# Optimization experiments

Measured on AMD Instinct MI355X. Metric: run time of the kernel, lower is better.

Reference implementation:

```python
import jax, jax.numpy as jnp
import numpy as np

N = 64
K_CHEB = 5
EPS = 1e-5

# db4 decomposition filters (scaling_filter.mat Lo_D / Hi_D, length 8)
_LO = np.array([-0.010597401784997278, 0.032883011666982945, 0.030841381835986965,
                -0.18703481171888114, -0.02798376941698385, 0.6308807679295904,
                0.7148465705525415, 0.23037781330885523], dtype=np.float32)
_HI = np.array([-0.23037781330885523, 0.7148465705525415, -0.6308807679295904,
                -0.02798376941698385, 0.18703481171888114, 0.030841381835986965,
                0.032883011666982945, -0.010597401784997278], dtype=np.float32)
# torch stores np.flip(filters) and Conv2d does cross-correlation -> use flipped taps here too
_KERN = np.stack([_LO[::-1], _HI[::-1]])[:, None, None, :].copy()  # [2,1,1,8]


def _wavelet_step(x):
    # x: [B, C, 1, W]; circular pad 3 each side, depthwise len-8 conv, stride 2
    p = 3  # filter_length // 2 - 1
    xp = jnp.concatenate([x[..., -p:], x, x[..., :p]], axis=-1)
    b, c, h, wp = xp.shape
    out = jax.lax.conv_general_dilated(
        xp.reshape(b * c, 1, h, wp), jnp.asarray(_KERN), (1, 2), 'VALID',
        dimension_numbers=('NCHW', 'OIHW', 'NCHW'))
    out = out.reshape(b, c, 2, h, -1)
    return out[:, :, 0], out[:, :, 1]  # (approx, detail)


def _cbam(x, fc1, fc2, sa_w):
    # x: [B, 657, 1, 64]; channel attention then spatial attention
    def mlp(v):  # v: [B, C, 1, 1]
        h = jax.nn.relu(jnp.einsum('oc,bchw->bohw', fc1, v))
        return jnp.einsum('oc,bchw->bohw', fc2, h)
    avg = x.mean(axis=(2, 3), keepdims=True)
    mx = x.max(axis=(2, 3), keepdims=True)
    x = x * jax.nn.sigmoid(mlp(avg) + mlp(mx))
    s = jnp.concatenate([x.mean(axis=1, keepdims=True), x.max(axis=1, keepdims=True)], axis=1)
    sa = jax.nn.sigmoid(jax.lax.conv_general_dilated(
        s, sa_w, (1, 1), ((3, 3), (3, 3)), dimension_numbers=('NCHW', 'OIHW', 'NCHW')))
    return x * sa


def _global_edge_weight(w_tril, mask):
    xs, ys = np.tril_indices(N)
    E = jnp.zeros((N, N), w_tril.dtype).at[xs, ys].set(w_tril)
    E = E + E.T - jnp.diag(jnp.diag(E))
    return (E * mask).reshape(-1)


def _norm_adj(edges, w):
    # PyG NewSGConv.norm: add remaining self-loops (fill=1), deg from |w|, sym normalize
    row, col = edges[0], edges[1]
    has_self = jnp.zeros((N,), w.dtype).at[row].add(jnp.where(row == col, 1.0, 0.0)) > 0
    w_self = jnp.where(has_self, 0.0, 1.0).astype(w.dtype)
    deg = jnp.zeros((N,), w.dtype).at[row].add(jnp.abs(w)) + w_self
    dsafe = jnp.where(deg > 0, deg, 1.0)
    dinv = jnp.where(deg > 0, jax.lax.rsqrt(dsafe), 0.0)
    norm = dinv[row] * w * dinv[col]
    A = jnp.zeros((N, N), w.dtype).at[col, row].add(norm)  # out[i] = sum_j A[i,j] x[j]
    return A + jnp.diag(dinv * w_self * dinv)


def _gcn_block(x, A, W, b, g, be):
    # x: [B, N, C_in]; K-hop SGConv propagation, linear, train-mode batchnorm over (B, N)
    for _ in range(K_CHEB):
        x = jnp.einsum('ij,bjc->bic', A, x)
    x = x @ W.T + b
    mean = x.mean(axis=(0, 1))
    var = x.var(axis=(0, 1))
    return (x - mean) * jax.lax.rsqrt(var + EPS) * g + be


def _classify(x, W1, b1, g, be, W2, b2):
    out = x.reshape(x.shape[0], -1) @ W1.T + b1
    out = (out - out.mean(0)) * jax.lax.rsqrt(out.var(0) + EPS) * g + be
    return jax.nn.log_softmax(out @ W2.T + b2, axis=1)


def _forward(x, local_graph_weight, global_mask, ca_fc1, ca_fc2, sa_conv, edge_weight_tril,
             ld_W, ld_b, ld_g, ld_be, ld1_W, ld1_b, ld1_g, ld1_be,
             d_W, d_b, d_g, d_be, d1_W, d1_b, d1_g, d1_be,
             cls_W1, cls_b1, cls_g, cls_be, cls_W2, cls_b2, edges):
    xc = jnp.transpose(x, (0, 3, 2, 1))        # [B, 657, 1, 64]
    xc = _cbam(xc, ca_fc1, ca_fc2, sa_conv)
    xh = jnp.transpose(xc, (0, 3, 2, 1))       # [B, 64, 1, 657]
    # fi = floor(log2(200)) = 7 -> 4 decomposition levels: 657->328->164->82->41
    out1, _gamma = _wavelet_step(xh)
    out2, _beta = _wavelet_step(out1)
    out3, _alpha = _wavelet_step(out2)
    delta, _theta = _wavelet_step(out3)        # [B, 64, 1, 41]
    delta = delta[:, :, 0, :]                  # squeeze -> [B, 64, 41]
    gw = _global_edge_weight(edge_weight_tril, global_mask)
    A_loc = _norm_adj(edges, local_graph_weight)
    A_glb = _norm_adj(edges, gw)
    lf = _gcn_block(delta, A_loc, ld_W, ld_b, ld_g, ld_be)
    lf = _gcn_block(lf, A_loc, ld1_W, ld1_b, ld1_g, ld1_be)
    gf = _gcn_block(delta, A_glb, d_W, d_b, d_g, d_be)
    gf = _gcn_block(gf, A_glb, d1_W, d1_b, d1_g, d1_be)
    feat = jnp.concatenate([lf.mean(-1, keepdims=True), gf.mean(-1, keepdims=True)], axis=2)  # [B,64,2]
    return _classify(feat, cls_W1, cls_b1, cls_g, cls_be, cls_W2, cls_b2)


def setup_inputs() -> dict:
    key = jax.random.key(0)
    ks = iter(jax.random.split(key, 16))
    B = 512
    f32 = jnp.float32
    def rn(shape, s=0.05):
        return jax.random.normal(next(ks), shape, f32) * s
    ii = jnp.arange(N, dtype=jnp.int32)
    edges = jnp.stack([jnp.repeat(ii, N), jnp.tile(ii, N)])  # full 64x64 mesh (incl. self loops)
    return dict(
        x=jax.random.normal(next(ks), (B, N, 1, 657), f32),
        local_graph_weight=jax.random.uniform(next(ks), (N * N,), f32),
        global_mask=jnp.ones((N, N), f32),
        ca_fc1=rn((82, 657)),
        ca_fc2=rn((657, 82)),
        sa_conv=rn((1, 2, 7, 7), 0.1),
        edge_weight_tril=jax.random.uniform(next(ks), (N * (N + 1) // 2,), f32),
        ld_W=rn((16, 41)), ld_b=jnp.zeros(16, f32), ld_g=jnp.ones(16, f32), ld_be=jnp.zeros(16, f32),
        ld1_W=rn((4, 16)), ld1_b=jnp.zeros(4, f32), ld1_g=jnp.ones(4, f32), ld1_be=jnp.zeros(4, f32),
        d_W=rn((16, 41)), d_b=jnp.zeros(16, f32), d_g=jnp.ones(16, f32), d_be=jnp.zeros(16, f32),
        d1_W=rn((4, 16)), d1_b=jnp.zeros(4, f32), d1_g=jnp.ones(4, f32), d1_be=jnp.zeros(4, f32),
        cls_W1=rn((32, 128)), cls_b1=jnp.zeros(32, f32), cls_g=jnp.ones(32, f32), cls_be=jnp.zeros(32, f32),
        cls_W2=rn((2, 32)), cls_b2=jnp.zeros(2, f32),
        edges=edges,
    )


def reference(x, local_graph_weight, global_mask, ca_fc1, ca_fc2, sa_conv, edge_weight_tril,
              ld_W, ld_b, ld_g, ld_be, ld1_W, ld1_b, ld1_g, ld1_be,
              d_W, d_b, d_g, d_be, d1_W, d1_b, d1_g, d1_be,
              cls_W1, cls_b1, cls_g, cls_be, cls_W2, cls_b2, edges):
    return _forward(x, local_graph_weight, global_mask, ca_fc1, ca_fc2, sa_conv, edge_weight_tril,
                    ld_W, ld_b, ld_g, ld_be, ld1_W, ld1_b, ld1_g, ld1_be,
                    d_W, d_b, d_g, d_be, d1_W, d1_b, d1_g, d1_be,
                    cls_W1, cls_b1, cls_g, cls_be, cls_W2, cls_b2, edges)
```

## Files before the change

kernel.cpp:

```cpp
#include <hip/hip_runtime.h>
#include <math.h>

#define NB 512
#define NN 64
#define TL 657
#define LV1 328
#define LV2 164
#define LV3 82
#define LV4 41
#define HID 82
#define ST 66
#define NGB 32

#define WS_M      0
#define WS_ACC    32768
#define WS_SMEAN  36864
#define WS_SMAX   167936
#define WS_CATT   3373568
#define WS_Y1     682496
#define WS_DELTA  4876800
#define WS_Y2     4876800
#define WS_OUT1   5925376

#define ACC_Y1 0
#define ACC_Y2 64
#define ACC_O1 80

__device__ __forceinline__ float sigmoidf_(float v){ return 1.0f/(1.0f+expf(-v)); }

__device__ __forceinline__ void wav_level(float* __restrict__ dst, const float* __restrict__ src,
                                          int outL, int inL, int lane){
  const float DLO[8] = {0.23037781330885523f, 0.7148465705525415f, 0.6308807679295904f,
                        -0.02798376941698385f, -0.18703481171888114f, 0.030841381835986965f,
                        0.032883011666982945f, -0.010597401784997278f};
  for (int k=lane; k<outL; k+=64){
    int i0 = 2*k - 3;
    float a = 0.f;
    #pragma unroll
    for (int j=0;j<8;j++){
      int idx = i0 + j;
      idx = (idx < 0) ? idx + inL : ((idx >= inL) ? idx - inL : idx);
      a += src[idx]*DLO[j];
    }
    dst[k] = a;
  }
}

__global__ __launch_bounds__(512) void k_front(
    const float* __restrict__ x,
    const float* __restrict__ lgw, const float* __restrict__ gmask,
    const float* __restrict__ tril, const int* __restrict__ edges,
    const float* __restrict__ fc1, const float* __restrict__ fc2,
    float* __restrict__ catt_g,
    float* __restrict__ Mout, double* __restrict__ acc)
{
  __shared__ float smem[8848];
  __shared__ float deg[64], hsv[64], dinv[64], wself[64];
  int tid = threadIdx.x;
  int bid = blockIdx.x;
  int wv = tid>>6, lane = tid&63;

  if (bid < NGB){
    int g  = bid >> 4;
    int s4 = (bid & 15) * 4;
    float* Wbuf = smem;
    float* Amat = smem + 4096;
    float* Rc   = smem + 8320;
    float* Rn   = smem + 8584;
    if (bid==0 && tid<512) acc[tid]=0.0;
    for (int e=tid;e<4096;e+=512){
      float w;
      if (g==0) w = lgw[e];
      else {
        int i=e>>6, j=e&63;
        int aa = (i>j)? i:j, bb = (i>j)? j:i;
        w = tril[aa*(aa+1)/2 + bb] * gmask[e];
      }
      Wbuf[e] = w;
    }
    for (int i=tid;i<NN*ST;i+=512) Amat[i] = 0.f;
    if (tid<64){ deg[tid]=0.f; hsv[tid]=0.f; }
    __syncthreads();
    {
      int e0 = tid*8;
      int runr = edges[e0];
      float runv = 0.f;
      #pragma unroll
      for (int i=0;i<8;i++){
        int e = e0+i;
        int r = edges[e];
        int c = edges[4096+e];
        float w = Wbuf[e];
        if (r != runr){ atomicAdd(&deg[runr], runv); runr = r; runv = 0.f; }
        runv += fabsf(w);
        if (r == c) hsv[r] = 1.f;
      }
      atomicAdd(&deg[runr], runv);
    }
    __syncthreads();
    if (tid<64){
      float w_ = (hsv[tid] > 0.f) ? 0.f : 1.f;
      float d = deg[tid] + w_;
      dinv[tid] = (d > 0.f) ? rsqrtf(d) : 0.f;
      wself[tid] = w_;
    }
    __syncthreads();
    for (int e=tid;e<4096;e+=512){
      int r = edges[e], c = edges[4096+e];
      float nm = dinv[r]*Wbuf[e]*dinv[c];
      atomicAdd(&Amat[c*ST+r], nm);
    }
    __syncthreads();
    if (tid<64) Amat[tid*ST+tid] += dinv[tid]*wself[tid]*dinv[tid];
    __syncthreads();
    if (tid < 256){
      int r = tid>>6, c = tid&63;
      Rc[r*ST+c] = Amat[(s4+r)*ST+c];
    }
    __syncthreads();
    #pragma unroll
    for (int it=0; it<4; it++){
      if (tid < 256){
        int r = tid>>6, c = tid&63;
        const float* rr = &Rc[r*ST];
        float a0=0.f, a1=0.f;
        #pragma unroll 8
        for (int k=0;k<64;k+=2){
          a0 += rr[k]  *Amat[k*ST+c];
          a1 += rr[k+1]*Amat[(k+1)*ST+c];
        }
        Rn[r*ST+c] = a0+a1;
      }
      __syncthreads();
      float* t = Rc; Rc = Rn; Rn = t;
    }
    if (tid < 256){
      int r = tid>>6, c = tid&63;
      Mout[g*4096 + (s4+r)*64 + c] = Rc[r*ST+c];
    }
    return;
  }

  int b = bid - NGB;
  const float4* xb4 = (const float4*)(x + (size_t)b*NN*TL);
  int f0 = tid;
  int f1 = 512 + tid;
  bool has1 = (f1 < 657);
  float4 S0 = make_float4(0.f,0.f,0.f,0.f);
  float4 M0 = make_float4(-INFINITY,-INFINITY,-INFINITY,-INFINITY);
  float4 S1 = S0, M1 = M0;
  #pragma unroll 4
  for (int g=0; g<16; ++g){
    float4 v = xb4[g*657 + f0];
    S0.x += v.x; S0.y += v.y; S0.z += v.z; S0.w += v.w;
    M0.x = fmaxf(M0.x, v.x); M0.y = fmaxf(M0.y, v.y);
    M0.z = fmaxf(M0.z, v.z); M0.w = fmaxf(M0.w, v.w);
    if (has1){
      float4 w = xb4[g*657 + f1];
      S1.x += w.x; S1.y += w.y; S1.z += w.z; S1.w += w.w;
      M1.x = fmaxf(M1.x, w.x); M1.y = fmaxf(M1.y, w.y);
      M1.z = fmaxf(M1.z, w.z); M1.w = fmaxf(M1.w, w.w);
    }
  }
  float* Sf = smem;
  float* Mf = smem + 2628;
  float* cs = smem + 5256;
  float* cm = smem + 5916;
  float* h  = smem + 6576;
  *(float4*)&Sf[4*f0] = S0;
  *(float4*)&Mf[4*f0] = M0;
  if (has1){
    *(float4*)&Sf[4*f1] = S1;
    *(float4*)&Mf[4*f1] = M1;
  }
  __syncthreads();
  for (int c=tid; c<TL; c+=512){
    cs[c] = (Sf[c] + Sf[c+657]) + (Sf[c+1314] + Sf[c+1971]);
    cm[c] = fmaxf(fmaxf(Mf[c], Mf[c+657]), fmaxf(Mf[c+1314], Mf[c+1971]));
  }
  __syncthreads();
  for (int o=wv; o<HID; o+=8){
    const float* fr = fc1 + (size_t)o*TL;
    float a = 0.f, bm = 0.f;
    #pragma unroll
    for (int i=0;i<11;i++){
      int c = lane + 64*i;
      if (c < TL){
        float f = fr[c];
        a += f*cs[c]; bm += f*cm[c];
      }
    }
    #pragma unroll
    for (int off=32;off;off>>=1){
      a  += __shfl_xor(a,off);
      bm += __shfl_xor(bm,off);
    }
    if (lane==0)
      h[o] = fmaxf(a*(1.0f/64.0f),0.f) + fmaxf(bm,0.f);
  }
  __syncthreads();
  for (int c=tid; c<TL; c+=512){
    const float2* fr = (const float2*)(fc2 + (size_t)c*HID);
    float a0=0.f, a1=0.f;
    #pragma unroll
    for (int u2=0;u2<41;u2++){
      float2 v = fr[u2];
      a0 += v.x*h[2*u2]; a1 += v.y*h[2*u2+1];
    }
    catt_g[(size_t)b*TL + c] = sigmoidf_(a0+a1);
  }
}

__global__ __launch_bounds__(256) void k_wav(
    const float* __restrict__ x, const float* __restrict__ catt_g,
    float* __restrict__ delta, float* __restrict__ smean, float* __restrict__ smax)
{
  __shared__ float catt[660];
  __shared__ float buf[2664];
  __shared__ float o1b[4][332];
  __shared__ float o2b[4][166];
  __shared__ float o3b[4][84];
  int tid = threadIdx.x, b = blockIdx.x, q = blockIdx.y;
  for (int i=tid;i<TL;i+=256) catt[i] = catt_g[(size_t)b*TL + i];
  __syncthreads();
  const float4* g4 = (const float4*)(x + ((size_t)b*NN + q*4)*TL);
  for (int f=tid; f<657; f+=256){
    float4 v = g4[f];
    int e = 4*f;
    if (f==164 || f==328 || f==492){
      float ev[4] = {v.x, v.y, v.z, v.w};
      #pragma unroll
      for (int j=0;j<4;j++){
        int ee = e+j;
        int r = (ee>=657) + (ee>=1314) + (ee>=1971);
        buf[ee + 12*r] = ev[j];
      }
    } else {
      int r = (e>=657) + (e>=1314) + (e>=1971);
      *(float4*)&buf[e + 12*r] = v;
    }
  }
  __syncthreads();
  int wv = tid>>6, lane = tid&63;
  int n = q*4 + wv;
  float* y = &buf[669*wv];
  float ls = 0.f, lm = -INFINITY;
  #pragma unroll
  for (int i=0;i<11;i++){
    int t = lane + 64*i;
    if (t < TL){
      float vv = y[t]*catt[t];
      y[t] = vv; ls += vv; lm = fmaxf(lm,vv);
    }
  }
  #pragma unroll
  for (int off=32;off;off>>=1){
    ls += __shfl_xor(ls,off);
    lm = fmaxf(lm, __shfl_xor(lm,off));
  }
  if (lane==0){ smean[b*NN+n] = ls*(1.0f/657.0f); smax[b*NN+n] = lm; }
  wav_level(o1b[wv], y,       LV1, TL,  lane);
  wav_level(o2b[wv], o1b[wv], LV2, LV1, lane);
  wav_level(o3b[wv], o2b[wv], LV3, LV2, lane);
  if (lane < LV4){
    const float DLO[8] = {0.23037781330885523f, 0.7148465705525415f, 0.6308807679295904f,
                          -0.02798376941698385f, -0.18703481171888114f, 0.030841381835986965f,
                          0.032883011666982945f, -0.010597401784997278f};
    int i0 = 2*lane - 3;
    float a = 0.f;
    #pragma unroll
    for (int j=0;j<8;j++){
      int idx = i0 + j;
      idx = (idx < 0) ? idx + LV3 : ((idx >= LV3) ? idx - LV3 : idx);
      a += o3b[wv][idx]*DLO[j];
    }
    delta[((size_t)b*NN + n)*LV4 + lane] = a;
  }
}

__global__ __launch_bounds__(256) void k_gcn1(
  const float* __restrict__ delta, const float* __restrict__ Mmat,
  const float* __restrict__ smean, const float* __restrict__ smax,
  const float* __restrict__ saw,
  const float* __restrict__ ldW, const float* __restrict__ ldb,
  const float* __restrict__ dW, const float* __restrict__ db2,
  float* __restrict__ Y1, double* __restrict__ acc)
{
  __shared__ float Dl[NN*LV4];
  __shared__ float Tt[NN*16];
  __shared__ float Mm[4096];
  __shared__ float Wl[16*LV4];
  __shared__ float satt[NN];
  __shared__ double red[256];
  int tid=threadIdx.x, b=blockIdx.x;
  if (tid < NN){
    float a = 0.f;
    #pragma unroll
    for (int kw=0;kw<7;kw++){
      int w = tid + kw - 3;
      if (0<=w && w<NN) a += smean[b*NN+w]*saw[21+kw] + smax[b*NN+w]*saw[70+kw];
    }
    satt[tid] = sigmoidf_(a);
  }
  __syncthreads();
  const float* ds = delta + (size_t)b*NN*LV4;
  for (int i=tid;i<NN*LV4;i+=256) Dl[i] = ds[i]*satt[i/LV4];
  for (int g=0; g<2; g++){
    const float* Ws = g ? dW : ldW;
    const float* bs = g ? db2 : ldb;
    for (int i=tid;i<16*LV4;i+=256) Wl[i]=Ws[i];
    const float4* Mm4 = (const float4*)(Mmat + g*4096);
    for (int i=tid;i<1024;i+=256) *(float4*)&Mm[4*i] = Mm4[i];
    __syncthreads();
    for (int e=tid;e<NN*16;e+=256){
      int n=e>>4, o=e&15;
      const float* dr=&Dl[n*LV4];
      const float* wr=&Wl[o*LV4];
      float a=0.f;
      #pragma unroll 8
      for (int c=0;c<LV4;c++) a += dr[c]*wr[c];
      Tt[e]=a;
    }
    __syncthreads();
    float bias = bs[tid&15];
    float ps=0.f, pq=0.f;
    for (int m=0;m<4;m++){
      int e=tid+256*m;
      int n=e>>4, o=e&15;
      float a=bias;
      #pragma unroll 8
      for (int k=0;k<64;k++) a += Mm[n*64+k]*Tt[k*16+o];
      Y1[((size_t)b*NN+n)*32 + g*16 + o] = a;
      ps += a; pq += a*a;
    }
    red[tid]=(double)ps;
    __syncthreads();
    if (tid<16){ double t=0; for (int r=tid;r<256;r+=16) t+=red[r]; atomicAdd(&acc[ACC_Y1+g*32+tid], t); }
    __syncthreads();
    red[tid]=(double)pq;
    __syncthreads();
    if (tid<16){ double t=0; for (int r=tid;r<256;r+=16) t+=red[r]; atomicAdd(&acc[ACC_Y1+g*32+16+tid], t); }
    __syncthreads();
  }
}

__global__ __launch_bounds__(256) void k_gcn2(
  const float* __restrict__ Y1, const float* __restrict__ Mmat,
  const float* __restrict__ ldg, const float* __restrict__ ldbe,
  const float* __restrict__ dg, const float* __restrict__ dbe,
  const float* __restrict__ ld1W, const float* __restrict__ ld1b,
  const float* __restrict__ d1W, const float* __restrict__ d1b,
  float* __restrict__ Y2, double* __restrict__ acc)
{
  __shared__ float Yl[NN*32];
  __shared__ float T2[NN*8];
  __shared__ float Mm[2*4096];
  __shared__ float scl[32], sht[32];
  __shared__ double red[256];
  int tid=threadIdx.x, b=blockIdx.x;
  const float4* ys4 = (const float4*)(Y1 + (size_t)b*NN*32);
  for (int i=tid;i<512;i+=256) *(float4*)&Yl[4*i] = ys4[i];
  const float4* Mm4 = (const float4*)Mmat;
  for (int i=tid;i<2048;i+=256) *(float4*)&Mm[4*i] = Mm4[i];
  if (tid<32){
    int g=tid>>4, o=tid&15;
    double s=acc[ACC_Y1+g*32+o], q=acc[ACC_Y1+g*32+16+o];
    double mean=s/32768.0;
    double var=q/32768.0 - mean*mean;
    float gam = g? dg[o] : ldg[o];
    float bet = g? dbe[o] : ldbe[o];
    float sc = gam * rsqrtf((float)var + 1e-5f);
    scl[tid]=sc; sht[tid]=bet - (float)mean*sc;
  }
  __syncthreads();
  for (int i=tid;i<NN*32;i+=256){ int c=i&31; Yl[i]=Yl[i]*scl[c]+sht[c]; }
  __syncthreads();
  for (int e=tid;e<NN*8;e+=256){
    int n=e>>3, c=e&7, g=c>>2, p=c&3;
    const float* w = (g? d1W : ld1W) + p*16;
    const float* yr = &Yl[n*32 + g*16];
    float a=0.f;
    #pragma unroll
    for (int o=0;o<16;o++) a += yr[o]*w[o];
    T2[e]=a;
  }
  __syncthreads();
  float ps=0.f,pq=0.f;
  for (int m=0;m<2;m++){
    int e=tid+256*m;
    int n=e>>3, c=e&7, g=c>>2;
    float a = g? d1b[c&3] : ld1b[c&3];
    const float* mr=&Mm[g*4096+n*64];
    #pragma unroll 8
    for (int k=0;k<64;k++) a += mr[k]*T2[k*8+c];
    Y2[((size_t)b*NN+n)*8 + c] = a;
    ps+=a; pq+=a*a;
  }
  red[tid]=(double)ps; __syncthreads();
  if (tid<8){ double t=0; for (int r=tid;r<256;r+=8) t+=red[r]; atomicAdd(&acc[ACC_Y2 + (tid>>2)*8 + (tid&3)], t); }
  __syncthreads();
  red[tid]=(double)pq; __syncthreads();
  if (tid<8){ double t=0; for (int r=tid;r<256;r+=8) t+=red[r]; atomicAdd(&acc[ACC_Y2 + (tid>>2)*8 + 4 + (tid&3)], t); }
}

__global__ __launch_bounds__(64) void k_featcls(
  const float* __restrict__ Y2,
  const float* __restrict__ ld1g, const float* __restrict__ ld1be,
  const float* __restrict__ d1g, const float* __restrict__ d1be,
  const float* __restrict__ W1, const float* __restrict__ b1,
  float* __restrict__ out1, double* __restrict__ acc)
{
  __shared__ float f[128];
  __shared__ float scl[8], sht[8];
  int tid=threadIdx.x, b=blockIdx.x;
  if (tid<8){
    int g=tid>>2, p=tid&3;
    double s=acc[ACC_Y2+g*8+p], q=acc[ACC_Y2+g*8+4+p];
    double mean=s/32768.0;
    double var=q/32768.0-mean*mean;
    float gam = g? d1g[p]:ld1g[p];
    float bet = g? d1be[p]:ld1be[p];
    float sc = gam*rsqrtf((float)var+1e-5f);
    scl[tid]=sc; sht[tid]=bet-(float)mean*sc;
  }
  __syncthreads();
  {
    const float* yr = Y2 + ((size_t)b*NN+tid)*8;
    float lf=0.f, gf=0.f;
    #pragma unroll
    for (int p=0;p<4;p++){
      lf += yr[p]*scl[p]+sht[p];
      gf += yr[4+p]*scl[4+p]+sht[4+p];
    }
    f[2*tid]   = lf*0.25f;
    f[2*tid+1] = gf*0.25f;
  }
  __syncthreads();
  if (tid<32){
    const float* w = W1 + tid*128;
    float a = b1[tid];
    #pragma unroll 4
    for (int m=0;m<128;m++) a += w[m]*f[m];
    out1[b*32+tid]=a;
    atomicAdd(&acc[ACC_O1+tid], (double)a);
    atomicAdd(&acc[ACC_O1+32+tid], (double)(a*a));
  }
}

__global__ __launch_bounds__(64) void k_cls2(
  const float* __restrict__ out1,
  const float* __restrict__ cg, const float* __restrict__ cbe,
  const float* __restrict__ W2, const float* __restrict__ b2,
  const double* __restrict__ acc, float* __restrict__ out)
{
  __shared__ float v[32];
  __shared__ float z[2];
  int tid=threadIdx.x, b=blockIdx.x;
  if (tid<32){
    double s=acc[ACC_O1+tid], q=acc[ACC_O1+32+tid];
    double mean=s/512.0;
    double var=q/512.0-mean*mean;
    float sc=cg[tid]*rsqrtf((float)var+1e-5f);
    float sh=cbe[tid]-(float)mean*sc;
    v[tid]=out1[b*32+tid]*sc+sh;
  }
  __syncthreads();
  if (tid<2){
    const float* w=W2+tid*32;
    float a=b2[tid];
    #pragma unroll
    for (int j=0;j<32;j++) a += w[j]*v[j];
    z[tid]=a;
  }
  __syncthreads();
  if (tid<2){
    float m=fmaxf(z[0],z[1]);
    float l=m+logf(expf(z[0]-m)+expf(z[1]-m));
    out[b*2+tid]=z[tid]-l;
  }
}

extern "C" void kernel_launch(void* const* d_in, const int* in_sizes, int n_in,
                              void* d_out, int out_size, void* d_ws, size_t ws_size,
                              hipStream_t stream) {
  (void)in_sizes; (void)n_in; (void)out_size; (void)ws_size;
  const float* x     = (const float*)d_in[0];
  const float* lgw   = (const float*)d_in[1];
  const float* gmask = (const float*)d_in[2];
  const float* fc1   = (const float*)d_in[3];
  const float* fc2   = (const float*)d_in[4];
  const float* saw   = (const float*)d_in[5];
  const float* tril  = (const float*)d_in[6];
  const float* ldW   = (const float*)d_in[7];
  const float* ldb   = (const float*)d_in[8];
  const float* ldg   = (const float*)d_in[9];
  const float* ldbe  = (const float*)d_in[10];
  const float* ld1W  = (const float*)d_in[11];
  const float* ld1b  = (const float*)d_in[12];
  const float* ld1g  = (const float*)d_in[13];
  const float* ld1be = (const float*)d_in[14];
  const float* dW    = (const float*)d_in[15];
  const float* db2   = (const float*)d_in[16];
  const float* dg    = (const float*)d_in[17];
  const float* dbe   = (const float*)d_in[18];
  const float* d1W   = (const float*)d_in[19];
  const float* d1b   = (const float*)d_in[20];
  const float* d1g   = (const float*)d_in[21];
  const float* d1be  = (const float*)d_in[22];
  const float* cW1   = (const float*)d_in[23];
  const float* cb1   = (const float*)d_in[24];
  const float* cgam  = (const float*)d_in[25];
  const float* cbet  = (const float*)d_in[26];
  const float* cW2   = (const float*)d_in[27];
  const float* cb2   = (const float*)d_in[28];
  const int*   edges = (const int*)d_in[29];

  char* ws = (char*)d_ws;
  float*  M     = (float*)(ws + WS_M);
  double* acc   = (double*)(ws + WS_ACC);
  float*  smean = (float*)(ws + WS_SMEAN);
  float*  smax  = (float*)(ws + WS_SMAX);
  float*  catt  = (float*)(ws + WS_CATT);
  float*  Y1    = (float*)(ws + WS_Y1);
  float*  delta = (float*)(ws + WS_DELTA);
  float*  Y2    = (float*)(ws + WS_Y2);
  float*  out1  = (float*)(ws + WS_OUT1);
  float*  out   = (float*)d_out;

  k_front<<<NB + NGB, 512, 0, stream>>>(x, lgw, gmask, tril, edges, fc1, fc2,
                                        catt, M, acc);
  k_wav<<<dim3(NB, 16), 256, 0, stream>>>(x, catt, delta, smean, smax);
  k_gcn1<<<NB, 256, 0, stream>>>(delta, M, smean, smax, saw, ldW, ldb, dW, db2, Y1, acc);
  k_gcn2<<<NB, 256, 0, stream>>>(Y1, M, ldg, ldbe, dg, dbe, ld1W, ld1b, d1W, d1b, Y2, acc);
  k_featcls<<<NB, 64, 0, stream>>>(Y2, ld1g, ld1be, d1g, d1be, cW1, cb1, out1, acc);
  k_cls2<<<NB, 64, 0, stream>>>(out1, cgam, cbet, cW2, cb2, acc, out);
}
```

Baseline: 168.2 us.

## Split channel-stat reduction across two blocks per batch with atomics and separate MLP kernel

The per-batch channel sum/max reduction over 64 rows is split across two blocks, each handling half the rows and combining results through global atomicAdd and atomicMax on order-preserving encoded floats. The channel-attention MLP moves into a new kernel that reads the combined stats. The goal is more parallelism for the memory-bound front reduction. In exchange it adds a memset, an extra kernel launch, atomic traffic, and float-sum order nondeterminism.

```diff
diff --git a/kernel.cpp b/kernel.cpp
--- a/kernel.cpp
+++ b/kernel.cpp
@@ -16,8 +16,10 @@
 #define WS_ACC    32768
 #define WS_SMEAN  36864
 #define WS_SMAX   167936
-#define WS_CATT   3373568
-#define WS_Y1     682496
+#define WS_CSUM   299008
+#define WS_CMAXU  1644544
+#define WS_CATT   2990080
+#define WS_Y1     299008
 #define WS_DELTA  4876800
 #define WS_Y2     4876800
 #define WS_OUT1   5925376
@@ -27,6 +29,15 @@
 #define ACC_O1 80
 
 __device__ __forceinline__ float sigmoidf_(float v){ return 1.0f/(1.0f+expf(-v)); }
+
+__device__ __forceinline__ unsigned fenc(float f){
+  unsigned u = __float_as_uint(f);
+  return (u & 0x80000000u) ? ~u : (u | 0x80000000u);
+}
+__device__ __forceinline__ float fdec(unsigned u){
+  unsigned v = (u & 0x80000000u) ? (u & 0x7fffffffu) : ~u;
+  return __uint_as_float(v);
+}
 
 __device__ __forceinline__ void wav_level(float* __restrict__ dst, const float* __restrict__ src,
                                           int outL, int inL, int lane){
@@ -46,19 +57,17 @@
   }
 }
 
-__global__ __launch_bounds__(512) void k_front(
+__global__ __launch_bounds__(512) void k_stats(
     const float* __restrict__ x,
     const float* __restrict__ lgw, const float* __restrict__ gmask,
     const float* __restrict__ tril, const int* __restrict__ edges,
-    const float* __restrict__ fc1, const float* __restrict__ fc2,
-    float* __restrict__ catt_g,
+    float* __restrict__ csum, unsigned* __restrict__ cmaxu,
     float* __restrict__ Mout, double* __restrict__ acc)
 {
   __shared__ float smem[8848];
   __shared__ float deg[64], hsv[64], dinv[64], wself[64];
   int tid = threadIdx.x;
   int bid = blockIdx.x;
-  int wv = tid>>6, lane = tid&63;
 
   if (bid < NGB){
     int g  = bid >> 4;
@@ -141,16 +150,17 @@
     return;
   }
 
-  int b = bid - NGB;
-  const float4* xb4 = (const float4*)(x + (size_t)b*NN*TL);
+  int sid = bid - NGB;
+  int b = sid >> 1, split = sid & 1;
+  const float4* xb4 = (const float4*)(x + (size_t)b*NN*TL) + (size_t)split*8*657;
   int f0 = tid;
   int f1 = 512 + tid;
   bool has1 = (f1 < 657);
   float4 S0 = make_float4(0.f,0.f,0.f,0.f);
   float4 M0 = make_float4(-INFINITY,-INFINITY,-INFINITY,-INFINITY);
   float4 S1 = S0, M1 = M0;
-  #pragma unroll 4
-  for (int g=0; g<16; ++g){
+  #pragma unroll
+  for (int g=0; g<8; ++g){
     float4 v = xb4[g*657 + f0];
     S0.x += v.x; S0.y += v.y; S0.z += v.z; S0.w += v.w;
     M0.x = fmaxf(M0.x, v.x); M0.y = fmaxf(M0.y, v.y);
@@ -164,9 +174,6 @@
   }
   float* Sf = smem;
   float* Mf = smem + 2628;
-  float* cs = smem + 5256;
-  float* cm = smem + 5916;
-  float* h  = smem + 6576;
   *(float4*)&Sf[4*f0] = S0;
   *(float4*)&Mf[4*f0] = M0;
   if (has1){
@@ -175,8 +182,24 @@
   }
   __syncthreads();
   for (int c=tid; c<TL; c+=512){
-    cs[c] = (Sf[c] + Sf[c+657]) + (Sf[c+1314] + Sf[c+1971]);
-    cm[c] = fmaxf(fmaxf(Mf[c], Mf[c+657]), fmaxf(Mf[c+1314], Mf[c+1971]));
+    float s = (Sf[c] + Sf[c+657]) + (Sf[c+1314] + Sf[c+1971]);
+    float m = fmaxf(fmaxf(Mf[c], Mf[c+657]), fmaxf(Mf[c+1314], Mf[c+1971]));
+    atomicAdd(&csum[(size_t)b*TL + c], s);
+    atomicMax(&cmaxu[(size_t)b*TL + c], fenc(m));
+  }
+}
+
+__global__ __launch_bounds__(512) void k_mlp(
+    const float* __restrict__ csum, const unsigned* __restrict__ cmaxu,
+    const float* __restrict__ fc1, const float* __restrict__ fc2,
+    float* __restrict__ catt_g)
+{
+  __shared__ float cs[660], cm[660], h[84];
+  int tid = threadIdx.x, b = blockIdx.x;
+  int wv = tid>>6, lane = tid&63;
+  for (int c=tid; c<TL; c+=512){
+    cs[c] = csum[(size_t)b*TL + c];
+    cm[c] = fdec(cmaxu[(size_t)b*TL + c]);
   }
   __syncthreads();
   for (int o=wv; o<HID; o+=8){
@@ -516,19 +539,23 @@
   const int*   edges = (const int*)d_in[29];
 
   char* ws = (char*)d_ws;
-  float*  M     = (float*)(ws + WS_M);
-  double* acc   = (double*)(ws + WS_ACC);
-  float*  smean = (float*)(ws + WS_SMEAN);
-  float*  smax  = (float*)(ws + WS_SMAX);
-  float*  catt  = (float*)(ws + WS_CATT);
-  float*  Y1    = (float*)(ws + WS_Y1);
-  float*  delta = (float*)(ws + WS_DELTA);
-  float*  Y2    = (float*)(ws + WS_Y2);
-  float*  out1  = (float*)(ws + WS_OUT1);
-  float*  out   = (float*)d_out;
-
-  k_front<<<NB + NGB, 512, 0, stream>>>(x, lgw, gmask, tril, edges, fc1, fc2,
-                                        catt, M, acc);
+  float*    M     = (float*)(ws + WS_M);
+  double*   acc   = (double*)(ws + WS_ACC);
+  float*    smean = (float*)(ws + WS_SMEAN);
+  float*    smax  = (float*)(ws + WS_SMAX);
+  float*    csum  = (float*)(ws + WS_CSUM);
+  unsigned* cmaxu = (unsigned*)(ws + WS_CMAXU);
+  float*    catt  = (float*)(ws + WS_CATT);
+  float*    Y1    = (float*)(ws + WS_Y1);
+  float*    delta = (float*)(ws + WS_DELTA);
+  float*    Y2    = (float*)(ws + WS_Y2);
+  float*    out1  = (float*)(ws + WS_OUT1);
+  float*    out   = (float*)d_out;
+
+  hipMemsetAsync(ws + WS_CSUM, 0, 2*512*TL*sizeof(float), stream);
+  k_stats<<<NGB + 2*NB, 512, 0, stream>>>(x, lgw, gmask, tril, edges,
+                                          csum, cmaxu, M, acc);
+  k_mlp<<<NB, 512, 0, stream>>>(csum, cmaxu, fc1, fc2, catt);
   k_wav<<<dim3(NB, 16), 256, 0, stream>>>(x, catt, delta, smean, smax);
   k_gcn1<<<NB, 256, 0, stream>>>(delta, M, smean, smax, saw, ldW, ldb, dW, db2, Y1, acc);
   k_gcn2<<<NB, 256, 0, stream>>>(Y1, M, ldg, ldbe, dg, dbe, ld1W, ld1b, d1W, d1b, Y2, acc);
```

Result: slower. 175.1 us (+4.1%).

## Widen front kernel to 1024 threads with per-wave row reduction and reordered blocks

Applied to the files above, without the earlier changes.

The front kernel now launches 1024 threads per block. Each wave reduces 4 of the 64 channel rows with scalar loads, and the partial sums and maxima are combined through a shared-memory tree. The graph-propagation blocks are moved to the end of the grid so batch blocks start first, and the edge loops are retuned for 1024 threads. The aim is more memory parallelism and latency hiding in the channel-attention pooling. The cost is more register pressure, more barriers and lower occupancy per CU at 1024 threads.

```diff
diff --git a/kernel.cpp b/kernel.cpp
--- a/kernel.cpp
+++ b/kernel.cpp
@@ -46,7 +46,7 @@
   }
 }
 
-__global__ __launch_bounds__(512) void k_front(
+__global__ __launch_bounds__(1024) void k_front(
     const float* __restrict__ x,
     const float* __restrict__ lgw, const float* __restrict__ gmask,
     const float* __restrict__ tril, const int* __restrict__ edges,
@@ -54,21 +54,22 @@
     float* __restrict__ catt_g,
     float* __restrict__ Mout, double* __restrict__ acc)
 {
-  __shared__ float smem[8848];
+  __shared__ float smem[3*NN*ST];
   __shared__ float deg[64], hsv[64], dinv[64], wself[64];
   int tid = threadIdx.x;
   int bid = blockIdx.x;
   int wv = tid>>6, lane = tid&63;
 
-  if (bid < NGB){
-    int g  = bid >> 4;
-    int s4 = (bid & 15) * 4;
+  if (bid >= NB){
+    int gi = bid - NB;
+    int g  = gi >> 4;
+    int s4 = (gi & 15) * 4;
     float* Wbuf = smem;
     float* Amat = smem + 4096;
     float* Rc   = smem + 8320;
     float* Rn   = smem + 8584;
-    if (bid==0 && tid<512) acc[tid]=0.0;
-    for (int e=tid;e<4096;e+=512){
+    if (gi==0 && tid<512) acc[tid]=0.0;
+    for (int e=tid;e<4096;e+=1024){
       float w;
       if (g==0) w = lgw[e];
       else {
@@ -78,15 +79,15 @@
       }
       Wbuf[e] = w;
     }
-    for (int i=tid;i<NN*ST;i+=512) Amat[i] = 0.f;
+    for (int i=tid;i<NN*ST;i+=1024) Amat[i] = 0.f;
     if (tid<64){ deg[tid]=0.f; hsv[tid]=0.f; }
     __syncthreads();
     {
-      int e0 = tid*8;
+      int e0 = tid*4;
       int runr = edges[e0];
       float runv = 0.f;
       #pragma unroll
-      for (int i=0;i<8;i++){
+      for (int i=0;i<4;i++){
         int e = e0+i;
         int r = edges[e];
         int c = edges[4096+e];
@@ -105,7 +106,7 @@
       wself[tid] = w_;
     }
     __syncthreads();
-    for (int e=tid;e<4096;e+=512){
+    for (int e=tid;e<4096;e+=1024){
       int r = edges[e], c = edges[4096+e];
       float nm = dinv[r]*Wbuf[e]*dinv[c];
       atomicAdd(&Amat[c*ST+r], nm);
@@ -141,73 +142,84 @@
     return;
   }
 
-  int b = bid - NGB;
-  const float4* xb4 = (const float4*)(x + (size_t)b*NN*TL);
-  int f0 = tid;
-  int f1 = 512 + tid;
-  bool has1 = (f1 < 657);
-  float4 S0 = make_float4(0.f,0.f,0.f,0.f);
-  float4 M0 = make_float4(-INFINITY,-INFINITY,-INFINITY,-INFINITY);
-  float4 S1 = S0, M1 = M0;
-  #pragma unroll 4
-  for (int g=0; g<16; ++g){
-    float4 v = xb4[g*657 + f0];
-    S0.x += v.x; S0.y += v.y; S0.z += v.z; S0.w += v.w;
-    M0.x = fmaxf(M0.x, v.x); M0.y = fmaxf(M0.y, v.y);
-    M0.z = fmaxf(M0.z, v.z); M0.w = fmaxf(M0.w, v.w);
-    if (has1){
-      float4 w = xb4[g*657 + f1];
-      S1.x += w.x; S1.y += w.y; S1.z += w.z; S1.w += w.w;
-      M1.x = fmaxf(M1.x, w.x); M1.y = fmaxf(M1.y, w.y);
-      M1.z = fmaxf(M1.z, w.z); M1.w = fmaxf(M1.w, w.w);
-    }
-  }
-  float* Sf = smem;
-  float* Mf = smem + 2628;
-  float* cs = smem + 5256;
-  float* cm = smem + 5916;
-  float* h  = smem + 6576;
-  *(float4*)&Sf[4*f0] = S0;
-  *(float4*)&Mf[4*f0] = M0;
-  if (has1){
-    *(float4*)&Sf[4*f1] = S1;
-    *(float4*)&Mf[4*f1] = M1;
-  }
-  __syncthreads();
-  for (int c=tid; c<TL; c+=512){
-    cs[c] = (Sf[c] + Sf[c+657]) + (Sf[c+1314] + Sf[c+1971]);
-    cm[c] = fmaxf(fmaxf(Mf[c], Mf[c+657]), fmaxf(Mf[c+1314], Mf[c+1971]));
-  }
-  __syncthreads();
-  for (int o=wv; o<HID; o+=8){
-    const float* fr = fc1 + (size_t)o*TL;
-    float a = 0.f, bm = 0.f;
-    #pragma unroll
-    for (int i=0;i<11;i++){
-      int c = lane + 64*i;
-      if (c < TL){
-        float f = fr[c];
-        a += f*cs[c]; bm += f*cm[c];
-      }
-    }
-    #pragma unroll
-    for (int off=32;off;off>>=1){
-      a  += __shfl_xor(a,off);
-      bm += __shfl_xor(bm,off);
-    }
-    if (lane==0)
-      h[o] = fmaxf(a*(1.0f/64.0f),0.f) + fmaxf(bm,0.f);
-  }
-  __syncthreads();
-  for (int c=tid; c<TL; c+=512){
-    const float2* fr = (const float2*)(fc2 + (size_t)c*HID);
-    float a0=0.f, a1=0.f;
-    #pragma unroll
-    for (int u2=0;u2<41;u2++){
-      float2 v = fr[u2];
-      a0 += v.x*h[2*u2]; a1 += v.y*h[2*u2+1];
-    }
-    catt_g[(size_t)b*TL + c] = sigmoidf_(a0+a1);
+  int b = bid;
+  {
+    float s[11], m[11];
+    #pragma unroll
+    for (int i=0;i<11;i++){ s[i]=0.f; m[i]=-INFINITY; }
+    const float* xb = x + (size_t)b*NN*TL;
+    for (int r=0;r<4;r++){
+      const float* row = xb + (size_t)(wv*4 + r)*TL;
+      #pragma unroll
+      for (int i=0;i<11;i++){
+        int t = lane + 64*i;
+        if (t < TL){
+          float v = row[t];
+          s[i] += v; m[i] = fmaxf(m[i], v);
+        }
+      }
+    }
+    for (int step=8; step>=1; step>>=1){
+      if (wv >= step && wv < 2*step){
+        float* bs = smem + (wv-step)*1328;
+        #pragma unroll
+        for (int i=0;i<11;i++){
+          int t = lane + 64*i;
+          if (t<TL){ bs[t] = s[i]; bs[664+t] = m[i]; }
+        }
+      }
+      __syncthreads();
+      if (wv < step){
+        float* bs = smem + wv*1328;
+        #pragma unroll
+        for (int i=0;i<11;i++){
+          int t = lane + 64*i;
+          if (t<TL){ s[i] += bs[t]; m[i] = fmaxf(m[i], bs[664+t]); }
+        }
+      }
+      __syncthreads();
+    }
+    float* cs = smem;
+    float* cm = smem + 664;
+    float* h  = smem + 1400;
+    if (wv==0){
+      #pragma unroll
+      for (int i=0;i<11;i++){
+        int t = lane + 64*i;
+        if (t<TL){ cs[t] = s[i]; cm[t] = m[i]; }
+      }
+    }
+    __syncthreads();
+    for (int o=wv; o<HID; o+=16){
+      const float* fr = fc1 + (size_t)o*TL;
+      float a = 0.f, bm = 0.f;
+      #pragma unroll
+      for (int i=0;i<11;i++){
+        int c = lane + 64*i;
+        if (c < TL){
+          float f = fr[c];
+          a += f*cs[c]; bm += f*cm[c];
+        }
+      }
+      #pragma unroll
+      for (int off=32;off;off>>=1){
+        a  += __shfl_xor(a,off);
+        bm += __shfl_xor(bm,off);
+      }
+      if (lane==0)
+        h[o] = fmaxf(a*(1.0f/64.0f),0.f) + fmaxf(bm,0.f);
+    }
+    __syncthreads();
+    if (tid < TL){
+      const float2* fr = (const float2*)(fc2 + (size_t)tid*HID);
+      float a0=0.f, a1=0.f;
+      #pragma unroll
+      for (int u2=0;u2<41;u2++){
+        float2 v = fr[u2];
+        a0 += v.x*h[2*u2]; a1 += v.y*h[2*u2+1];
+      }
+      catt_g[(size_t)b*TL + tid] = sigmoidf_(a0+a1);
+    }
   }
 }
 
@@ -527,8 +539,8 @@
   float*  out1  = (float*)(ws + WS_OUT1);
   float*  out   = (float*)d_out;
 
-  k_front<<<NB + NGB, 512, 0, stream>>>(x, lgw, gmask, tril, edges, fc1, fc2,
-                                        catt, M, acc);
+  k_front<<<NB + NGB, 1024, 0, stream>>>(x, lgw, gmask, tril, edges, fc1, fc2,
+                                         catt, M, acc);
   k_wav<<<dim3(NB, 16), 256, 0, stream>>>(x, catt, delta, smean, smax);
   k_gcn1<<<NB, 256, 0, stream>>>(delta, M, smean, smax, saw, ldW, ldb, dW, db2, Y1, acc);
   k_gcn2<<<NB, 256, 0, stream>>>(Y1, M, ldg, ldbe, dg, dbe, ld1W, ld1b, d1W, d1b, Y2, acc);
```

Measured after the change: 166.5 us. Within noise of the previous version (-1.0%).
